# Kernel tuning notes

Measured on AMD Instinct MI355X. Metric: run time of the kernel, lower is better.

## Reference

```python
import jax, jax.numpy as jnp
import numpy as np

N_NODES, E_TOT, E_ACT = 20000, 250000, 200000
LAT, OH = 128, 128
M0, M1, M2 = 64, 32, 16            # irreps_out: 64x0e + 32x1o + 16x2e
D_IR = M0 + 3 * M1 + 5 * M2        # 240
G = M1 + M2                        # gate scalars (48)
T0 = M0 + G                        # tp m=0 scalar channels (112)
I0, I1, I2 = 3 * M0, 3 * M1, 3 * M2  # tp input muls (center|edge|neighbor)


def _split(x, m0, m1, m2):
    e = x.shape[0]
    return (x[:, :m0],
            x[:, m0:m0 + 3 * m1].reshape(e, m1, 3),
            x[:, m0 + 3 * m1:].reshape(e, m2, 5))


def _merge(s0, s1, s2):
    e = s0.shape[0]
    return jnp.concatenate([s0, s1.reshape(e, -1), s2.reshape(e, -1)], axis=-1)


def _mlp(x, ws, bs):
    for i, (w, b) in enumerate(zip(ws, bs)):
        x = x @ w + b
        if i < len(ws) - 1:
            x = jax.nn.silu(x)
    return x


def _forward(latents, node_features, edge_features, cutoff_coeffs, edge_one_hot,
             wigner_D1, wigner_D2,
             W0, W1r, W1i, W2r, W2i, Gw, Gb,
             P0, P0b, P1, P2, Ew, Eb, ln_g, ln_b,
             A1, A1b, A2, A2b, A3, A3b,
             B1, B1b, B2, B2b, B3, B3b,
             O0, O1, O2,
             edge_index, active_edges):
    ec = edge_index[0][active_edges]
    en = edge_index[1][active_edges]
    # gather node features per edge (equivariant_norm_type='none' -> identity norms)
    nc0, nc1, nc2 = _split(node_features[ec], M0, M1, M2)
    ef0, ef1, ef2 = _split(edge_features, M0, M1, M2)
    nn0, nn1, nn2 = _split(node_features[en], M0, M1, M2)
    x0 = jnp.concatenate([nc0, ef0, nn0], -1)   # [E,192]
    x1 = jnp.concatenate([nc1, ef1, nn1], 1)    # [E,96,3]
    x2 = jnp.concatenate([nc2, ef2, nn2], 1)    # [E,48,5]
    lat_a = latents[active_edges]
    # --- SO(2) linear: rotate into edge frame, per-m mixing, latent gains, rotate back ---
    r1 = jnp.einsum('eij,euj->eui', wigner_D1, x1)
    r2 = jnp.einsum('eij,euj->eui', wigner_D2, x2)
    in0 = jnp.concatenate([x0, r1[:, :, 1], r2[:, :, 2]], -1)   # m=0 [E,336]
    o_m0 = in0 @ W0.T                                           # [E,160]
    ip1 = jnp.concatenate([r1[:, :, 2], r2[:, :, 3]], -1)       # m=+1 [E,144]
    im1 = jnp.concatenate([r1[:, :, 0], r2[:, :, 1]], -1)       # m=-1
    op1 = ip1 @ W1r.T - im1 @ W1i.T                             # [E,48]
    on1 = ip1 @ W1i.T + im1 @ W1r.T
    op2 = r2[:, :, 4] @ W2r.T - r2[:, :, 0] @ W2i.T             # [E,16]
    on2 = r2[:, :, 4] @ W2i.T + r2[:, :, 0] @ W2r.T
    g = lat_a @ Gw + Gb                                         # per-edge gains [E,224]
    o_m0 = o_m0 * g[:, :160]
    g1 = g[:, 160:208]; g2 = g[:, 208:224]
    op1 = op1 * g1; on1 = on1 * g1; op2 = op2 * g2; on2 = on2 * g2
    y0 = o_m0[:, :T0]
    y1 = jnp.stack([on1[:, :M1], o_m0[:, T0:T0 + M1], op1[:, :M1]], -1)          # [E,32,3]
    y2 = jnp.stack([on2, on1[:, M1:], o_m0[:, T0 + M1:], op1[:, M1:], op2], -1)  # [E,16,5]
    y1 = jnp.einsum('eji,euj->eui', wigner_D1, y1)
    y2 = jnp.einsum('eji,euj->eui', wigner_D2, y2)
    # --- gate activation ---
    gates = jax.nn.sigmoid(y0[:, M0:])
    z0 = jax.nn.silu(y0[:, :M0])
    z1 = y1 * gates[:, :M1, None]
    z2 = y2 * gates[:, M1:, None]
    # --- lin_post: per-l channel mixing, fan-in normalized, bias on scalars ---
    z0 = z0 @ P0.T / np.sqrt(M0) + P0b
    z1 = jnp.einsum('uv,evm->eum', P1, z1) / np.sqrt(M1)
    z2 = jnp.einsum('uv,evm->eum', P2, z2) / np.sqrt(M2)
    scalars = z0                                               # taken before weighting
    # --- E3ElementLinear: per-edge per-channel weights from latents ---
    w = lat_a @ Ew + Eb                                        # [E,112]
    z0 = z0 * w[:, :M0]
    z1 = z1 * w[:, M0:M0 + M1, None]
    z2 = z2 * w[:, M0 + M1:, None]
    new_edge = _merge(z0, z1, z2)
    # --- latent update: LN -> mlp1(ln_lat||scalars) -> mlp2(h||one_hot) -> cutoff ---
    mu = lat_a.mean(-1, keepdims=True)
    var = ((lat_a - mu) ** 2).mean(-1, keepdims=True)
    ln_lat = (lat_a - mu) * jax.lax.rsqrt(var + 1e-5) * ln_g + ln_b
    h = _mlp(jnp.concatenate([ln_lat, scalars], -1), (A1, A2, A3), (A1b, A2b, A3b))
    h = _mlp(jnp.concatenate([h, edge_one_hot], -1), (B1, B2, B3), (B1b, B2b, B3b))
    new_lat = cutoff_coeffs[active_edges][:, None] * h
    # --- residual update (res_update_params buffer = 0) ---
    u = jax.nn.sigmoid(jnp.asarray(0.0, new_edge.dtype))
    c_old = jax.lax.rsqrt(u * u + 1.0)
    c_new = u * c_old
    edge_out = c_old * edge_features + c_new * new_edge        # identity residual path
    latents_out = latents.at[active_edges].set(c_new * new_lat + c_old * lat_a)
    # --- layer one-hot tensor product (uvu with 128x0e) ---
    f0, f1, f2 = _split(edge_out, M0, M1, M2)
    s = 1.0 / np.sqrt(OH)
    t0 = f0 * (edge_one_hot @ O0.T) * s
    t1 = f1 * (edge_one_hot @ O1.T)[:, :, None] * s
    t2 = f2 * (edge_one_hot @ O2.T)[:, :, None] * s
    edge_out = edge_out + _merge(t0, t1, t2)
    return edge_out, latents_out


def setup_inputs() -> dict:
    key = jax.random.key(0)
    ks = iter(jax.random.split(key, 64))
    nrm = lambda sh, s=0.05: jax.random.normal(next(ks), sh, jnp.float32) * s
    inp = dict(
        latents=nrm((E_TOT, LAT), 1.0),
        node_features=nrm((N_NODES, D_IR), 1.0),
        edge_features=nrm((E_ACT, D_IR), 1.0),
        cutoff_coeffs=jax.random.uniform(next(ks), (E_TOT,), jnp.float32),
        edge_one_hot=jax.random.uniform(next(ks), (E_ACT, OH), jnp.float32),
        wigner_D1=nrm((E_ACT, 3, 3), 0.5),
        wigner_D2=nrm((E_ACT, 5, 5), 0.3),
        W0=nrm((160, I0 + I1 + I2)), W1r=nrm((48, 144)), W1i=nrm((48, 144)),
        W2r=nrm((16, 48)), W2i=nrm((16, 48)),
        Gw=nrm((LAT, 224)), Gb=jnp.ones((224,), jnp.float32),
        P0=nrm((M0, M0)), P0b=nrm((M0,)), P1=nrm((M1, M1)), P2=nrm((M2, M2)),
        Ew=nrm((LAT, M0 + M1 + M2)), Eb=jnp.ones((M0 + M1 + M2,), jnp.float32),
        ln_g=jnp.ones((LAT,), jnp.float32), ln_b=jnp.zeros((LAT,), jnp.float32),
        A1=nrm((LAT + M0, LAT)), A1b=nrm((LAT,)),
        A2=nrm((LAT, LAT)), A2b=nrm((LAT,)),
        A3=nrm((LAT, LAT)), A3b=nrm((LAT,)),
        B1=nrm((LAT + OH, LAT)), B1b=nrm((LAT,)),
        B2=nrm((LAT, LAT)), B2b=nrm((LAT,)),
        B3=nrm((LAT, LAT)), B3b=nrm((LAT,)),
        O0=nrm((M0, OH)), O1=nrm((M1, OH)), O2=nrm((M2, OH)),
        edge_index=jax.random.randint(next(ks), (2, E_TOT), 0, N_NODES, jnp.int32),
        active_edges=jnp.sort(jax.random.permutation(next(ks), E_TOT)[:E_ACT]).astype(jnp.int32),
    )
    return inp


def reference(latents, node_features, edge_features, cutoff_coeffs, edge_one_hot,
              wigner_D1, wigner_D2,
              W0, W1r, W1i, W2r, W2i, Gw, Gb,
              P0, P0b, P1, P2, Ew, Eb, ln_g, ln_b,
              A1, A1b, A2, A2b, A3, A3b,
              B1, B1b, B2, B2b, B3, B3b,
              O0, O1, O2, edge_index, active_edges):
    return _forward(latents, node_features, edge_features, cutoff_coeffs, edge_one_hot,
                    wigner_D1, wigner_D2,
                    W0, W1r, W1i, W2r, W2i, Gw, Gb,
                    P0, P0b, P1, P2, Ew, Eb, ln_g, ln_b,
                    A1, A1b, A2, A2b, A3, A3b,
                    B1, B1b, B2, B2b, B3, B3b,
                    O0, O1, O2, edge_index, active_edges)
```

## Files before the change

### kernel.cpp

```cpp
#include <hip/hip_runtime.h>

typedef unsigned short us_t;
typedef short bf16x8 __attribute__((ext_vector_type(8)));
typedef float f32x4 __attribute__((ext_vector_type(4)));

#define E_ACT 200000
#define E_TOT 250000
#define DIR   240
#define C_OLD 0.8944271909999159f
#define C_NEW 0.4472135954999579f
#define S_OH  0.08838834764831845f

#define WO_W0   0
#define WO_W1P  56320
#define WO_W1M  70144
#define WO_W2P  83968
#define WO_W2M  85504
#define WO_GW   87040
#define WO_EW   115712
#define WO_A1   130048
#define WO_A2   154624
#define WO_A3   171008
#define WO_B1   187392
#define WO_B2   220160
#define WO_B3   236544
#define WO_O0   252928
#define WO_O1   261120
#define WO_O2   265216
#define WO_P0T  267264
#define WO_P1T  271360
#define WO_P2T  272384
#define W_TOTAL 272896

__device__ __forceinline__ float b2f(us_t u) { return __uint_as_float(((unsigned)u) << 16); }
__device__ __forceinline__ us_t f2b(float f) {
    unsigned x = __float_as_uint(f);
    return (us_t)((x + 0x7fffu + ((x >> 16) & 1u)) >> 16);
}
__device__ __forceinline__ float sigm(float x) { return 1.0f / (1.0f + __expf(-x)); }

#define MFMA(a,b,c) __builtin_amdgcn_mfma_f32_16x16x32_bf16((a),(b),(c),0,0,0)

__global__ __launch_bounds__(256) void prep_kernel(
    const float* __restrict__ W0, const float* __restrict__ W1r, const float* __restrict__ W1i,
    const float* __restrict__ W2r, const float* __restrict__ W2i,
    const float* __restrict__ Gw, const float* __restrict__ Ew,
    const float* __restrict__ A1, const float* __restrict__ A2, const float* __restrict__ A3,
    const float* __restrict__ B1, const float* __restrict__ B2, const float* __restrict__ B3,
    const float* __restrict__ O0, const float* __restrict__ O1, const float* __restrict__ O2,
    const float* __restrict__ P0w, const float* __restrict__ P1w, const float* __restrict__ P2w,
    us_t* __restrict__ wb)
{
    int idx = blockIdx.x * 256 + threadIdx.x;
    if (idx >= W_TOTAL) return;
    float v;
    if (idx < WO_W1P) {
        int r = idx, n = r / 352, k = r % 352;
        v = (k < 336) ? W0[n * 336 + k] : 0.f;
    } else if (idx < WO_W1M) {
        int r = idx - WO_W1P, n = r / 288, k = r % 288;
        v = (k < 144) ? W1r[n * 144 + k] : -W1i[n * 144 + (k - 144)];
    } else if (idx < WO_W2P) {
        int r = idx - WO_W1M, n = r / 288, k = r % 288;
        v = (k < 144) ? W1i[n * 144 + k] : W1r[n * 144 + (k - 144)];
    } else if (idx < WO_W2M) {
        int r = idx - WO_W2P, n = r / 96, k = r % 96;
        v = (k < 48) ? W2r[n * 48 + k] : -W2i[n * 48 + (k - 48)];
    } else if (idx < WO_GW) {
        int r = idx - WO_W2M, n = r / 96, k = r % 96;
        v = (k < 48) ? W2i[n * 48 + k] : W2r[n * 48 + (k - 48)];
    } else if (idx < WO_EW) {
        int r = idx - WO_GW, n = r / 128, k = r % 128;
        v = Gw[k * 224 + n];
    } else if (idx < WO_A1) {
        int r = idx - WO_EW, n = r / 128, k = r % 128;
        v = Ew[k * 112 + n];
    } else if (idx < WO_A2) {
        int r = idx - WO_A1, n = r / 192, k = r % 192;
        v = A1[k * 128 + n];
    } else if (idx < WO_A3) {
        int r = idx - WO_A2, n = r / 128, k = r % 128;
        v = A2[k * 128 + n];
    } else if (idx < WO_B1) {
        int r = idx - WO_A3, n = r / 128, k = r % 128;
        v = A3[k * 128 + n];
    } else if (idx < WO_B2) {
        int r = idx - WO_B1, n = r / 256, k = r % 256;
        v = B1[k * 128 + n];
    } else if (idx < WO_B3) {
        int r = idx - WO_B2, n = r / 128, k = r % 128;
        v = B2[k * 128 + n];
    } else if (idx < WO_O0) {
        int r = idx - WO_B3, n = r / 128, k = r % 128;
        v = B3[k * 128 + n];
    } else if (idx < WO_O1) {
        v = O0[idx - WO_O0];
    } else if (idx < WO_O2) {
        v = O1[idx - WO_O1];
    } else if (idx < WO_P0T) {
        v = O2[idx - WO_O2];
    } else if (idx < WO_P1T) {
        v = P0w[idx - WO_P0T];
    } else if (idx < WO_P2T) {
        v = P1w[idx - WO_P1T];
    } else {
        int r = idx - WO_P2T, n = r / 32, k = r % 32;
        v = (k < 16) ? P2w[n * 16 + k] : 0.f;
    }
    wb[idx] = f2b(v);
}

__device__ __forceinline__ void lat_fetch_a(const float* __restrict__ latents,
                                            const int* __restrict__ aes_l,
                                            int lane, bf16x8 a[4])
{
    const int r = lane & 15, g = lane >> 4;
    const float* lp = latents + (size_t)aes_l[r] * 128 + g * 8;
    #pragma unroll
    for (int ks = 0; ks < 4; ++ks) {
        float4 v0 = *(const float4*)(lp + ks * 32);
        float4 v1 = *(const float4*)(lp + ks * 32 + 4);
        bf16x8 av;
        av[0] = (short)f2b(v0.x); av[1] = (short)f2b(v0.y);
        av[2] = (short)f2b(v0.z); av[3] = (short)f2b(v0.w);
        av[4] = (short)f2b(v1.x); av[5] = (short)f2b(v1.y);
        av[6] = (short)f2b(v1.z); av[7] = (short)f2b(v1.w);
        a[ks] = av;
    }
}

__device__ __forceinline__ void gemmW0g32(
    const us_t* __restrict__ in0s, const us_t* __restrict__ wbase,
    const bf16x8 lA[4], const bf16x8 lB[4], const float* __restrict__ Gb,
    int nt, us_t* __restrict__ om0g, int lane)
{
    const int r = lane & 15, g = lane >> 4;
    f32x4 wa = {0.f,0.f,0.f,0.f}, wb = wa, ga = wa, gb = wa;
    const us_t* apA = in0s + r * 360 + g * 8;
    const us_t* apB = in0s + (16 + r) * 360 + g * 8;
    const us_t* wp  = wbase + WO_W0 + (size_t)(nt * 16 + r) * 352 + g * 8;
    #pragma unroll
    for (int ks = 0; ks < 11; ++ks) {
        bf16x8 b = *(const bf16x8*)(wp + ks * 32);
        wa = MFMA(*(const bf16x8*)(apA + ks * 32), b, wa);
        wb = MFMA(*(const bf16x8*)(apB + ks * 32), b, wb);
    }
    const us_t* gp = wbase + WO_GW + (size_t)(nt * 16 + r) * 128 + g * 8;
    #pragma unroll
    for (int ks = 0; ks < 4; ++ks) {
        bf16x8 b = *(const bf16x8*)(gp + ks * 32);
        ga = MFMA(lA[ks], b, ga);
        gb = MFMA(lB[ks], b, gb);
    }
    float bi = Gb[nt * 16 + r];
    #pragma unroll
    for (int i = 0; i < 4; ++i) {
        int eA = g * 4 + i, eB = 16 + g * 4 + i;
        om0g[eA * 162 + nt * 16 + r] = f2b(wa[i] * (ga[i] + bi));
        om0g[eB * 162 + nt * 16 + r] = f2b(wb[i] * (gb[i] + bi));
    }
}

__device__ __forceinline__ void gemmW1g32(
    const us_t* __restrict__ cact1, const us_t* __restrict__ wbase,
    const bf16x8 lA[4], const bf16x8 lB[4], const float* __restrict__ Gb,
    int j, us_t* __restrict__ cp1g, us_t* __restrict__ cn1g, int lane)
{
    const int r = lane & 15, g = lane >> 4;
    f32x4 pa = {0.f,0.f,0.f,0.f}, pb = pa, ma = pa, mb = pa, ga = pa, gb = pa;
    const us_t* apA = cact1 + r * 296 + g * 8;
    const us_t* apB = cact1 + (16 + r) * 296 + g * 8;
    const us_t* wpP = wbase + WO_W1P + (size_t)(j * 16 + r) * 288 + g * 8;
    const us_t* wpM = wbase + WO_W1M + (size_t)(j * 16 + r) * 288 + g * 8;
    #pragma unroll
    for (int ks = 0; ks < 9; ++ks) {
        bf16x8 aA = *(const bf16x8*)(apA + ks * 32);
        bf16x8 aB = *(const bf16x8*)(apB + ks * 32);
        bf16x8 bP = *(const bf16x8*)(wpP + ks * 32);
        bf16x8 bM = *(const bf16x8*)(wpM + ks * 32);
        pa = MFMA(aA, bP, pa); pb = MFMA(aB, bP, pb);
        ma = MFMA(aA, bM, ma); mb = MFMA(aB, bM, mb);
    }
    const us_t* gp = wbase + WO_GW + (size_t)(160 + j * 16 + r) * 128 + g * 8;
    #pragma unroll
    for (int ks = 0; ks < 4; ++ks) {
        bf16x8 b = *(const bf16x8*)(gp + ks * 32);
        ga = MFMA(lA[ks], b, ga);
        gb = MFMA(lB[ks], b, gb);
    }
    float bi = Gb[160 + j * 16 + r];
    #pragma unroll
    for (int i = 0; i < 4; ++i) {
        int eA = g * 4 + i, eB = 16 + g * 4 + i;
        float gA = ga[i] + bi, gB = gb[i] + bi;
        cp1g[eA * 50 + j * 16 + r] = f2b(pa[i] * gA);
        cn1g[eA * 50 + j * 16 + r] = f2b(ma[i] * gA);
        cp1g[eB * 50 + j * 16 + r] = f2b(pb[i] * gB);
        cn1g[eB * 50 + j * 16 + r] = f2b(mb[i] * gB);
    }
}

__device__ __forceinline__ void gemmW2g32(
    const us_t* __restrict__ cact2, const us_t* __restrict__ wbase,
    const bf16x8 lA[4], const bf16x8 lB[4], const float* __restrict__ Gb,
    us_t* __restrict__ cp2g, us_t* __restrict__ cn2g, int lane)
{
    const int r = lane & 15, g = lane >> 4;
    f32x4 pa = {0.f,0.f,0.f,0.f}, pb = pa, ma = pa, mb = pa, ga = pa, gb = pa;
    const us_t* apA = cact2 + r * 104 + g * 8;
    const us_t* apB = cact2 + (16 + r) * 104 + g * 8;
    const us_t* wpP = wbase + WO_W2P + (size_t)r * 96 + g * 8;
    const us_t* wpM = wbase + WO_W2M + (size_t)r * 96 + g * 8;
    #pragma unroll
    for (int ks = 0; ks < 3; ++ks) {
        bf16x8 aA = *(const bf16x8*)(apA + ks * 32);
        bf16x8 aB = *(const bf16x8*)(apB + ks * 32);
        bf16x8 bP = *(const bf16x8*)(wpP + ks * 32);
        bf16x8 bM = *(const bf16x8*)(wpM + ks * 32);
        pa = MFMA(aA, bP, pa); pb = MFMA(aB, bP, pb);
        ma = MFMA(aA, bM, ma); mb = MFMA(aB, bM, mb);
    }
    const us_t* gp = wbase + WO_GW + (size_t)(208 + r) * 128 + g * 8;
    #pragma unroll
    for (int ks = 0; ks < 4; ++ks) {
        bf16x8 b = *(const bf16x8*)(gp + ks * 32);
        ga = MFMA(lA[ks], b, ga);
        gb = MFMA(lB[ks], b, gb);
    }
    float bi = Gb[208 + r];
    #pragma unroll
    for (int i = 0; i < 4; ++i) {
        int eA = g * 4 + i, eB = 16 + g * 4 + i;
        float gA = ga[i] + bi, gB = gb[i] + bi;
        cp2g[eA * 18 + r] = f2b(pa[i] * gA);
        cn2g[eA * 18 + r] = f2b(ma[i] * gA);
        cp2g[eB * 18 + r] = f2b(pb[i] * gB);
        cn2g[eB * 18 + r] = f2b(mb[i] * gB);
    }
}

__device__ __forceinline__ void lat_gemmE32(
    const bf16x8 lA[4], const bf16x8 lB[4],
    const us_t* __restrict__ wgt, const float* __restrict__ bias,
    int nt, us_t* __restrict__ wl, int lane)
{
    const int r = lane & 15, g = lane >> 4;
    f32x4 aA = {0.f,0.f,0.f,0.f}, aB = aA;
    const us_t* wp = wgt + (size_t)(nt * 16 + r) * 128 + g * 8;
    #pragma unroll
    for (int ks = 0; ks < 4; ++ks) {
        bf16x8 b = *(const bf16x8*)(wp + ks * 32);
        aA = MFMA(lA[ks], b, aA);
        aB = MFMA(lB[ks], b, aB);
    }
    float bi = bias[nt * 16 + r];
    #pragma unroll
    for (int i = 0; i < 4; ++i) {
        int eA = g * 4 + i, eB = 16 + g * 4 + i;
        wl[eA * 120 + nt * 16 + r] = f2b(aA[i] + bi);
        wl[eB * 120 + nt * 16 + r] = f2b(aB[i] + bi);
    }
}

template<int KS>
__device__ __forceinline__ void pgemm32(const us_t* __restrict__ actbase, int as,
                                        const us_t* __restrict__ wgt, int kp, int lane,
                                        f32x4& accA, f32x4& accB)
{
    const int r = lane & 15, g = lane >> 4;
    const us_t* apA = actbase + r * as + g * 8;
    const us_t* apB = actbase + (16 + r) * as + g * 8;
    const us_t* wp = wgt + (size_t)r * kp + g * 8;
    #pragma unroll
    for (int ks = 0; ks < KS; ++ks) {
        bf16x8 b = *(const bf16x8*)(wp + ks * 32);
        accA = MFMA(*(const bf16x8*)(apA + ks * 32), b, accA);
        accB = MFMA(*(const bf16x8*)(apB + ks * 32), b, accB);
    }
}

__global__ __launch_bounds__(256, 2) void k1_kernel(
    const float* __restrict__ latents,
    const float* __restrict__ node_features,
    const float* __restrict__ edge_features,
    const float* __restrict__ wD1,
    const float* __restrict__ wD2,
    const float* __restrict__ Gb,  const float* __restrict__ Eb,
    const float* __restrict__ P0b,
    const int* __restrict__ edge_index, const int* __restrict__ active_edges,
    const us_t* __restrict__ wbase,
    us_t* __restrict__ ne_ws, us_t* __restrict__ scal_ws)
{
    __shared__ __align__(16) char smem[80640];
    us_t* in0s  = (us_t*)(smem);
    us_t* cact1 = (us_t*)(smem + 23040);
    us_t* cact2 = (us_t*)(smem + 41984);
    float* D1l  = (float*)(smem + 48640);
    float* D2l  = (float*)(smem + 50176);
    int*   aes  = (int*)(smem + 53760);
    us_t* om0g  = (us_t*)(smem + 53888);
    us_t* cp1g  = (us_t*)(smem + 64256);
    us_t* cn1g  = (us_t*)(smem + 67456);
    us_t* cp2g  = (us_t*)(smem + 70656);
    us_t* cn2g  = (us_t*)(smem + 71808);
    us_t* wl    = (us_t*)(smem + 72960);
    us_t* z0l   = (us_t*)(smem);
    us_t* z1l   = (us_t*)(smem + 4608);
    us_t* z2l   = (us_t*)(smem + 11264);

    const int t  = threadIdx.x;
    const int e0 = blockIdx.x * 32;

    #pragma unroll
    for (int ep = 0; ep < 2; ++ep) {
        const int e = (t >> 4) + 16 * ep, l = t & 15;
        const int eg = e0 + e;
        const int ae = active_edges[eg];
        const int ec = edge_index[ae];
        const int en = edge_index[E_TOT + ae];
        if (l == 0) aes[e] = ae;

        float v1  = (l < 9) ? wD1[(size_t)eg * 9 + l] : 0.f;
        float v2a = wD2[(size_t)eg * 25 + l];
        float v2b = (l < 9) ? wD2[(size_t)eg * 25 + 16 + l] : 0.f;
        if (l < 9) D1l[e * 12 + l] = v1;
        D2l[e * 28 + l] = v2a;
        if (l < 9) D2l[e * 28 + 16 + l] = v2b;

        float d1[9], d2[25];
        #pragma unroll
        for (int i = 0; i < 9; ++i)  d1[i] = __shfl(v1, i, 16);
        #pragma unroll
        for (int i = 0; i < 16; ++i) d2[i] = __shfl(v2a, i, 16);
        #pragma unroll
        for (int i = 0; i < 9; ++i)  d2[16 + i] = __shfl(v2b, i, 16);

        const float* pc = node_features + (size_t)ec * DIR;
        const float* pe = edge_features + (size_t)eg * DIR;
        const float* pn = node_features + (size_t)en * DIR;
        us_t* in0 = in0s + e * 360;
        us_t* c1  = cact1 + e * 296;
        us_t* c2  = cact2 + e * 104;

        #pragma unroll
        for (int j = 0; j < 4; ++j) {
            int i = l + 16 * j;
            in0[i]       = f2b(pc[i]);
            in0[64 + i]  = f2b(pe[i]);
            in0[128 + i] = f2b(pn[i]);
        }
        in0[336 + l] = 0;

        #pragma unroll
        for (int jj = 0; jj < 6; ++jj) {
            int u = l + 16 * jj;
            int uu = u & 31;
            const float* sp = (u < 32 ? pc : (u < 64 ? pe : pn)) + 64 + uu * 3;
            float x0 = sp[0], x1 = sp[1], x2 = sp[2];
            float r0 = d1[0] * x0 + d1[1] * x1 + d1[2] * x2;
            float r1 = d1[3] * x0 + d1[4] * x1 + d1[5] * x2;
            float r2 = d1[6] * x0 + d1[7] * x1 + d1[8] * x2;
            c1[144 + u]  = f2b(r0);
            in0[192 + u] = f2b(r1);
            c1[u]        = f2b(r2);
        }
        #pragma unroll
        for (int jj = 0; jj < 3; ++jj) {
            int u = l + 16 * jj;
            int uu = u & 15;
            const float* sp = (u < 16 ? pc : (u < 32 ? pe : pn)) + 160 + uu * 5;
            float x0 = sp[0], x1 = sp[1], x2 = sp[2], x3 = sp[3], x4 = sp[4];
            float r[5];
            #pragma unroll
            for (int i = 0; i < 5; ++i)
                r[i] = d2[i * 5 + 0] * x0 + d2[i * 5 + 1] * x1 + d2[i * 5 + 2] * x2
                     + d2[i * 5 + 3] * x3 + d2[i * 5 + 4] * x4;
            c2[48 + u]   = f2b(r[0]);
            c1[240 + u]  = f2b(r[1]);
            in0[288 + u] = f2b(r[2]);
            c1[96 + u]   = f2b(r[3]);
            c2[u]        = f2b(r[4]);
        }
    }
    __syncthreads();

    {
        const int lane = t & 63, w = t >> 6;
        bf16x8 lA[4], lB[4];
        lat_fetch_a(latents, aes, lane, lA);
        lat_fetch_a(latents, aes + 16, lane, lB);
        if (w == 0) {
            gemmW0g32(in0s, wbase, lA, lB, Gb, 0, om0g, lane);
            gemmW0g32(in0s, wbase, lA, lB, Gb, 1, om0g, lane);
            gemmW0g32(in0s, wbase, lA, lB, Gb, 2, om0g, lane);
            gemmW1g32(cact1, wbase, lA, lB, Gb, 0, cp1g, cn1g, lane);
        } else if (w == 1) {
            gemmW0g32(in0s, wbase, lA, lB, Gb, 3, om0g, lane);
            gemmW0g32(in0s, wbase, lA, lB, Gb, 4, om0g, lane);
            gemmW0g32(in0s, wbase, lA, lB, Gb, 5, om0g, lane);
            gemmW1g32(cact1, wbase, lA, lB, Gb, 1, cp1g, cn1g, lane);
        } else if (w == 2) {
            gemmW0g32(in0s, wbase, lA, lB, Gb, 6, om0g, lane);
            gemmW0g32(in0s, wbase, lA, lB, Gb, 7, om0g, lane);
            gemmW0g32(in0s, wbase, lA, lB, Gb, 8, om0g, lane);
            gemmW1g32(cact1, wbase, lA, lB, Gb, 2, cp1g, cn1g, lane);
        } else {
            gemmW0g32(in0s, wbase, lA, lB, Gb, 9, om0g, lane);
            gemmW2g32(cact2, wbase, lA, lB, Gb, cp2g, cn2g, lane);
            #pragma unroll
            for (int nt = 0; nt < 7; ++nt)
                lat_gemmE32(lA, lB, wbase + WO_EW, Eb, nt, wl, lane);
        }
    }
    __syncthreads();

    #pragma unroll
    for (int ep = 0; ep < 2; ++ep) {
        const int e = (t >> 4) + 16 * ep, l = t & 15;
        const float* D1e = D1l + e * 12;
        const float* D2e = D2l + e * 28;
        #pragma unroll
        for (int uu = 0; uu < 2; ++uu) {
            int u = l + uu * 16;
            float j0 = b2f(cn1g[e * 50 + u]);
            float j1 = b2f(om0g[e * 162 + 112 + u]);
            float j2 = b2f(cp1g[e * 50 + u]);
            float gate = sigm(b2f(om0g[e * 162 + 64 + u]));
            #pragma unroll
            for (int i = 0; i < 3; ++i) {
                float yr = D1e[0 * 3 + i] * j0 + D1e[1 * 3 + i] * j1 + D1e[2 * 3 + i] * j2;
                z1l[e * 104 + i * 32 + u] = f2b(yr * gate);
            }
        }
        {
            int u = l;
            float j0 = b2f(cn2g[e * 18 + u]);
            float j1 = b2f(cn1g[e * 50 + 32 + u]);
            float j2 = b2f(om0g[e * 162 + 144 + u]);
            float j3 = b2f(cp1g[e * 50 + 32 + u]);
            float j4 = b2f(cp2g[e * 18 + u]);
            float gate = sigm(b2f(om0g[e * 162 + 96 + u]));
            #pragma unroll
            for (int i = 0; i < 5; ++i) {
                float yr = D2e[0 * 5 + i] * j0 + D2e[1 * 5 + i] * j1 + D2e[2 * 5 + i] * j2
                         + D2e[3 * 5 + i] * j3 + D2e[4 * 5 + i] * j4;
                z2l[e * 168 + i * 32 + u] = f2b(yr * gate);
                z2l[e * 168 + i * 32 + 16 + u] = 0;
            }
        }
        #pragma unroll
        for (int ii = 0; ii < 4; ++ii) {
            int c = l + 16 * ii;
            float v = b2f(om0g[e * 162 + c]);
            z0l[e * 72 + c] = f2b(v * sigm(v));
        }
    }
    __syncthreads();

    {
        const int lane = t & 63, w = t >> 6;
        const int r = lane & 15, g = lane >> 4;
        const float sc1 = 0.17677669529663687f;
        if (w < 2) {
            #pragma unroll
            for (int jj = 0; jj < 2; ++jj) {
                int nt = 2 * w + jj;
                f32x4 aA = {0.f,0.f,0.f,0.f}, aB = aA;
                pgemm32<2>(z0l, 72, wbase + WO_P0T + nt * 16 * 64, 64, lane, aA, aB);
                int n = nt * 16 + r;
                float bi = P0b[n];
                #pragma unroll
                for (int i = 0; i < 4; ++i) {
                    int eA = g * 4 + i, eB = 16 + g * 4 + i;
                    float zA = aA[i] * 0.125f + bi;
                    float zB = aB[i] * 0.125f + bi;
                    scal_ws[(size_t)(e0 + eA) * 64 + n] = f2b(zA);
                    scal_ws[(size_t)(e0 + eB) * 64 + n] = f2b(zB);
                    ne_ws[(size_t)(e0 + eA) * 240 + n] = f2b(zA * b2f(wl[eA * 120 + n]));
                    ne_ws[(size_t)(e0 + eB) * 240 + n] = f2b(zB * b2f(wl[eB * 120 + n]));
                }
            }
        } else if (w == 2) {
            #pragma unroll
            for (int m = 0; m < 3; ++m) {
                #pragma unroll
                for (int nt = 0; nt < 2; ++nt) {
                    f32x4 aA = {0.f,0.f,0.f,0.f}, aB = aA;
                    pgemm32<1>(z1l + m * 32, 104, wbase + WO_P1T + nt * 16 * 32, 32,
                               lane, aA, aB);
                    int u = nt * 16 + r;
                    #pragma unroll
                    for (int i = 0; i < 4; ++i) {
                        int eA = g * 4 + i, eB = 16 + g * 4 + i;
                        ne_ws[(size_t)(e0 + eA) * 240 + 64 + u * 3 + m] =
                            f2b(aA[i] * sc1 * b2f(wl[eA * 120 + 64 + u]));
                        ne_ws[(size_t)(e0 + eB) * 240 + 64 + u * 3 + m] =
                            f2b(aB[i] * sc1 * b2f(wl[eB * 120 + 64 + u]));
                    }
                }
            }
        } else if (w == 3) {
            #pragma unroll
            for (int m = 0; m < 5; ++m) {
                f32x4 aA = {0.f,0.f,0.f,0.f}, aB = aA;
                pgemm32<1>(z2l + m * 32, 168, wbase + WO_P2T, 32, lane, aA, aB);
                int u = r;
                #pragma unroll
                for (int i = 0; i < 4; ++i) {
                    int eA = g * 4 + i, eB = 16 + g * 4 + i;
                    ne_ws[(size_t)(e0 + eA) * 240 + 160 + u * 5 + m] =
                        f2b(aA[i] * 0.25f * b2f(wl[eA * 120 + 96 + u]));
                    ne_ws[(size_t)(e0 + eB) * 240 + 160 + u * 5 + m] =
                        f2b(aB[i] * 0.25f * b2f(wl[eB * 120 + 96 + u]));
                }
            }
        }
    }
}

template<int KS, bool SILU>
__device__ __forceinline__ void mlayer(
    const us_t* __restrict__ actA, const us_t* __restrict__ actB, int split, int as,
    const us_t* __restrict__ wgt, int kp, const float* __restrict__ bias,
    us_t* __restrict__ out, int os, int lane, int w)
{
    const int r = lane & 15, g = lane >> 4;
    const int n0 = 2 * w * 16, n1 = n0 + 16;
    f32x4 a00 = {0.f,0.f,0.f,0.f}, a01 = a00, a10 = a00, a11 = a00;
    const us_t* wp0 = wgt + (size_t)(n0 + r) * kp + g * 8;
    const us_t* wp1 = wgt + (size_t)(n1 + r) * kp + g * 8;
    #pragma unroll
    for (int ks = 0; ks < KS; ++ks) {
        const us_t* ab = (ks < split) ? (actA + ks * 32) : (actB + (ks - split) * 32);
        bf16x8 f0 = *(const bf16x8*)(ab + r * as + g * 8);
        bf16x8 f1 = *(const bf16x8*)(ab + (16 + r) * as + g * 8);
        bf16x8 b0 = *(const bf16x8*)(wp0 + ks * 32);
        bf16x8 b1 = *(const bf16x8*)(wp1 + ks * 32);
        a00 = MFMA(f0, b0, a00); a01 = MFMA(f0, b1, a01);
        a10 = MFMA(f1, b0, a10); a11 = MFMA(f1, b1, a11);
    }
    float bi0 = bias[n0 + r], bi1 = bias[n1 + r];
    #pragma unroll
    for (int i = 0; i < 4; ++i) {
        int eA = g * 4 + i, eB = 16 + g * 4 + i;
        float v;
        v = a00[i] + bi0; if (SILU) v *= sigm(v); out[eA * os + n0 + r] = f2b(v);
        v = a01[i] + bi1; if (SILU) v *= sigm(v); out[eA * os + n1 + r] = f2b(v);
        v = a10[i] + bi0; if (SILU) v *= sigm(v); out[eB * os + n0 + r] = f2b(v);
        v = a11[i] + bi1; if (SILU) v *= sigm(v); out[eB * os + n1 + r] = f2b(v);
    }
}

__global__ __launch_bounds__(256, 3) void k2_kernel(
    const float* __restrict__ latents, const float* __restrict__ cutoff,
    const float* __restrict__ one_hot,
    const float* __restrict__ ln_g, const float* __restrict__ ln_b,
    const float* __restrict__ A1b, const float* __restrict__ A2b, const float* __restrict__ A3b,
    const float* __restrict__ B1b, const float* __restrict__ B2b, const float* __restrict__ B3b,
    const int* __restrict__ active_edges,
    const us_t* __restrict__ wbase,
    const us_t* __restrict__ scal_ws, us_t* __restrict__ ohw_ws,
    float* __restrict__ out_lat)
{
    __shared__ __align__(16) char smem[39424];
    us_t* x_lds = (us_t*)(smem);
    us_t* h_a   = (us_t*)(smem + 12800);
    us_t* h_b   = (us_t*)(smem + 21504);
    us_t* ohl   = (us_t*)(smem + 30208);
    int*  aes_l = (int*)(smem + 38912);
    float* cut_l= (float*)(smem + 39040);

    const int t  = threadIdx.x;
    const int e0 = blockIdx.x * 32;
    const int lane = t & 63, w = t >> 6;

    {
        int ee = t >> 3, l8 = t & 7;
        int ae = active_edges[e0 + ee];
        if (l8 == 0) { aes_l[ee] = ae; cut_l[ee] = cutoff[ae]; }
        const float* lp = latents + (size_t)ae * 128 + l8 * 16;
        float xs[16];
        #pragma unroll
        for (int q = 0; q < 4; ++q) {
            float4 v = *(const float4*)(lp + q * 4);
            xs[q * 4 + 0] = v.x; xs[q * 4 + 1] = v.y;
            xs[q * 4 + 2] = v.z; xs[q * 4 + 3] = v.w;
        }
        float s1 = 0.f, s2 = 0.f;
        #pragma unroll
        for (int i = 0; i < 16; ++i) { s1 += xs[i]; s2 += xs[i] * xs[i]; }
        #pragma unroll
        for (int off = 1; off < 8; off <<= 1) {
            s1 += __shfl_xor(s1, off, 8);
            s2 += __shfl_xor(s2, off, 8);
        }
        float mu  = s1 * (1.f / 128.f);
        float var = s2 * (1.f / 128.f) - mu * mu;
        float rstd = rsqrtf(var + 1e-5f);
        #pragma unroll
        for (int i = 0; i < 16; ++i) {
            int li = l8 * 16 + i;
            x_lds[ee * 200 + li] = f2b((xs[i] - mu) * rstd * ln_g[li] + ln_b[li]);
        }
    }
    for (int idx = t; idx < 32 * 16; idx += 256) {
        int ee = idx >> 4, j = idx & 15;
        *(ushort4*)&x_lds[ee * 200 + 128 + j * 4] =
            *(const ushort4*)&scal_ws[(size_t)(e0 + ee) * 64 + j * 4];
    }
    for (int idx = t; idx < 32 * 32; idx += 256) {
        int ee = idx >> 5, j = idx & 31;
        float4 ov = *(const float4*)&one_hot[(size_t)(e0 + ee) * 128 + j * 4];
        ushort4 s; s.x = f2b(ov.x); s.y = f2b(ov.y); s.z = f2b(ov.z); s.w = f2b(ov.w);
        *(ushort4*)&ohl[ee * 136 + j * 4] = s;
    }
    __syncthreads();

    mlayer<6, true>(x_lds, x_lds, 6, 200, wbase + WO_A1, 192, A1b, h_a, 136, lane, w);
    __syncthreads();
    mlayer<4, true>(h_a, h_a, 4, 136, wbase + WO_A2, 128, A2b, h_b, 136, lane, w);
    __syncthreads();
    mlayer<4, false>(h_b, h_b, 4, 136, wbase + WO_A3, 128, A3b, h_a, 136, lane, w);
    __syncthreads();
    mlayer<8, true>(h_a, ohl, 4, 136, wbase + WO_B1, 256, B1b, h_b, 136, lane, w);
    __syncthreads();
    mlayer<4, true>(h_b, h_b, 4, 136, wbase + WO_B2, 128, B2b, h_a, 136, lane, w);
    __syncthreads();
    {
        const int r = lane & 15, g = lane >> 4;
        const int n0 = 2 * w * 16, n1 = n0 + 16;
        f32x4 a00 = {0.f,0.f,0.f,0.f}, a01 = a00, a10 = a00, a11 = a00;
        const us_t* wp0 = wbase + WO_B3 + (size_t)(n0 + r) * 128 + g * 8;
        const us_t* wp1 = wbase + WO_B3 + (size_t)(n1 + r) * 128 + g * 8;
        #pragma unroll
        for (int ks = 0; ks < 4; ++ks) {
            bf16x8 f0 = *(const bf16x8*)(h_a + ks * 32 + r * 136 + g * 8);
            bf16x8 f1 = *(const bf16x8*)(h_a + ks * 32 + (16 + r) * 136 + g * 8);
            bf16x8 b0 = *(const bf16x8*)(wp0 + ks * 32);
            bf16x8 b1 = *(const bf16x8*)(wp1 + ks * 32);
            a00 = MFMA(f0, b0, a00); a01 = MFMA(f0, b1, a01);
            a10 = MFMA(f1, b0, a10); a11 = MFMA(f1, b1, a11);
        }
        float bi0 = B3b[n0 + r], bi1 = B3b[n1 + r];
        #pragma unroll
        for (int i = 0; i < 4; ++i) {
            int eA = g * 4 + i, eB = 16 + g * 4 + i;
            int aeA = aes_l[eA], aeB = aes_l[eB];
            float cA = C_NEW * cut_l[eA], cB = C_NEW * cut_l[eB];
            float* oA = out_lat + (size_t)aeA * 128;
            float* oB = out_lat + (size_t)aeB * 128;
            const float* lA = latents + (size_t)aeA * 128;
            const float* lB = latents + (size_t)aeB * 128;
            oA[n0 + r] = cA * (a00[i] + bi0) + C_OLD * lA[n0 + r];
            oA[n1 + r] = cA * (a01[i] + bi1) + C_OLD * lA[n1 + r];
            oB[n0 + r] = cB * (a10[i] + bi0) + C_OLD * lB[n0 + r];
            oB[n1 + r] = cB * (a11[i] + bi1) + C_OLD * lB[n1 + r];
        }
    }

    {
        const int r = lane & 15, g = lane >> 4;
        const int cnt = (w == 3) ? 1 : 2;
        #pragma unroll
        for (int ii = 0; ii < 2; ++ii) {
            if (ii >= cnt) break;
            int nt = (ii == 0) ? w : w + 4;
            const us_t* wb2 = (nt < 4) ? (wbase + WO_O0 + (size_t)nt * 16 * 128)
                            : (nt < 6) ? (wbase + WO_O1 + (size_t)(nt - 4) * 16 * 128)
                                       : (wbase + WO_O2);
            f32x4 c0 = {0.f,0.f,0.f,0.f}, c1 = c0;
            const us_t* wp = wb2 + (size_t)r * 128 + g * 8;
            #pragma unroll
            for (int ks = 0; ks < 4; ++ks) {
                bf16x8 f0 = *(const bf16x8*)(ohl + ks * 32 + r * 136 + g * 8);
                bf16x8 f1 = *(const bf16x8*)(ohl + ks * 32 + (16 + r) * 136 + g * 8);
                bf16x8 b = *(const bf16x8*)(wp + ks * 32);
                c0 = MFMA(f0, b, c0); c1 = MFMA(f1, b, c1);
            }
            int n = nt * 16 + r;
            #pragma unroll
            for (int i = 0; i < 4; ++i) {
                int eA = e0 + g * 4 + i, eB = e0 + 16 + g * 4 + i;
                ohw_ws[(size_t)eA * 112 + n] = f2b(c0[i]);
                ohw_ws[(size_t)eB * 112 + n] = f2b(c1[i]);
            }
        }
    }
}

__global__ __launch_bounds__(256) void kfin_kernel(
    const float* __restrict__ edge_features, const us_t* __restrict__ ne_ws,
    const us_t* __restrict__ ohw_ws, float* __restrict__ out_edge)
{
    int idx = blockIdx.x * 256 + threadIdx.x;
    if (idx >= E_ACT * 60) return;
    int e = idx / 60;
    int c0 = (idx - e * 60) * 4;
    float4 ef = *(const float4*)&edge_features[(size_t)e * 240 + c0];
    ushort4 nv = *(const ushort4*)&ne_ws[(size_t)e * 240 + c0];
    float nef[4] = {b2f(nv.x), b2f(nv.y), b2f(nv.z), b2f(nv.w)};
    float eff[4] = {ef.x, ef.y, ef.z, ef.w};
    float4 ov;
    float* op = &ov.x;
    #pragma unroll
    for (int j = 0; j < 4; ++j) {
        int c = c0 + j;
        int o;
        if (c < 64)       o = c;
        else if (c < 160) o = 64 + (c - 64) / 3;
        else              o = 96 + (c - 160) / 5;
        float ohv = b2f(ohw_ws[(size_t)e * 112 + o]);
        op[j] = (C_OLD * eff[j] + C_NEW * nef[j]) * (1.f + S_OH * ohv);
    }
    *(float4*)&out_edge[(size_t)e * 240 + c0] = ov;
}

extern "C" void kernel_launch(void* const* d_in, const int* in_sizes, int n_in,
                              void* d_out, int out_size, void* d_ws, size_t ws_size,
                              hipStream_t stream)
{
    const float* latents  = (const float*)d_in[0];
    const float* node_f   = (const float*)d_in[1];
    const float* edge_f   = (const float*)d_in[2];
    const float* cutoff   = (const float*)d_in[3];
    const float* one_hot  = (const float*)d_in[4];
    const float* wD1      = (const float*)d_in[5];
    const float* wD2      = (const float*)d_in[6];
    const float* W0       = (const float*)d_in[7];
    const float* W1r      = (const float*)d_in[8];
    const float* W1i      = (const float*)d_in[9];
    const float* W2r      = (const float*)d_in[10];
    const float* W2i      = (const float*)d_in[11];
    const float* Gw       = (const float*)d_in[12];
    const float* Gb       = (const float*)d_in[13];
    const float* P0w      = (const float*)d_in[14];
    const float* P0b      = (const float*)d_in[15];
    const float* P1w      = (const float*)d_in[16];
    const float* P2w      = (const float*)d_in[17];
    const float* Ew       = (const float*)d_in[18];
    const float* Eb       = (const float*)d_in[19];
    const float* ln_g     = (const float*)d_in[20];
    const float* ln_b     = (const float*)d_in[21];
    const float* A1       = (const float*)d_in[22];
    const float* A1b      = (const float*)d_in[23];
    const float* A2       = (const float*)d_in[24];
    const float* A2b      = (const float*)d_in[25];
    const float* A3       = (const float*)d_in[26];
    const float* A3b      = (const float*)d_in[27];
    const float* B1       = (const float*)d_in[28];
    const float* B1b      = (const float*)d_in[29];
    const float* B2       = (const float*)d_in[30];
    const float* B2b      = (const float*)d_in[31];
    const float* B3       = (const float*)d_in[32];
    const float* B3b      = (const float*)d_in[33];
    const float* O0       = (const float*)d_in[34];
    const float* O1       = (const float*)d_in[35];
    const float* O2       = (const float*)d_in[36];
    const int* edge_index = (const int*)d_in[37];
    const int* act_e      = (const int*)d_in[38];

    float* out_edge = (float*)d_out;
    float* out_lat  = out_edge + (size_t)E_ACT * DIR;

    us_t* ne_ws   = (us_t*)d_ws;
    us_t* ohw_ws  = ne_ws + (size_t)E_ACT * DIR;
    us_t* scal_ws = ohw_ws + (size_t)E_ACT * 112;
    us_t* wbase   = scal_ws + (size_t)E_ACT * 64;

    prep_kernel<<<dim3((W_TOTAL + 255) / 256), dim3(256), 0, stream>>>(
        W0, W1r, W1i, W2r, W2i, Gw, Ew, A1, A2, A3, B1, B2, B3,
        O0, O1, O2, P0w, P1w, P2w, wbase);

    hipMemcpyAsync(out_lat, latents, (size_t)E_TOT * 128 * sizeof(float),
                   hipMemcpyDeviceToDevice, stream);

    k1_kernel<<<dim3(E_ACT / 32), dim3(256), 0, stream>>>(
        latents, node_f, edge_f, wD1, wD2, Gb, Eb, P0b,
        edge_index, act_e, wbase, ne_ws, scal_ws);

    k2_kernel<<<dim3(E_ACT / 32), dim3(256), 0, stream>>>(
        latents, cutoff, one_hot, ln_g, ln_b,
        A1b, A2b, A3b, B1b, B2b, B3b,
        act_e, wbase, scal_ws, ohw_ws, out_lat);

    kfin_kernel<<<dim3((E_ACT * 60 + 255) / 256), dim3(256), 0, stream>>>(
        edge_f, ne_ws, ohw_ws, out_edge);
}
```

Before: 713.6 us.

## Tile latent MLP at 64 edges per block and copy only inactive latent rows

The latent MLP kernel now handles 64 edges per block instead of 32. Each wave reuses its weight fragments across four row groups, which doubles MFMA work per weight load but needs twice the LDS and lowers occupancy to 2 blocks. The full-tensor device copy of latents into the output is replaced by a kernel that binary-searches the active edge list and copies only inactive rows, so rows that k2 overwrites are no longer written twice. The binary search adds per-thread scattered reads of the index array.

New measurement: 718.3 us. Within noise of the previous version (+0.7%).

```diff
diff --git a/kernel.cpp b/kernel.cpp
--- a/kernel.cpp
+++ b/kernel.cpp
@@ -110,6 +110,27 @@
     wb[idx] = f2b(v);
 }
 
+__global__ __launch_bounds__(256) void kcopy_kernel(
+    const float* __restrict__ latents, const int* __restrict__ act,
+    float* __restrict__ out_lat)
+{
+    int idx = blockIdx.x * 256 + threadIdx.x;
+    if (idx >= E_TOT * 16) return;
+    int row = idx >> 4, part = idx & 15;
+    int lo = 0, hi = E_ACT;
+    while (lo < hi) {
+        int mid = (lo + hi) >> 1;
+        if (act[mid] < row) lo = mid + 1; else hi = mid;
+    }
+    bool active = (lo < E_ACT) && (act[lo] == row);
+    if (!active) {
+        const float4* src = (const float4*)&latents[(size_t)row * 128 + part * 8];
+        float4* dst = (float4*)&out_lat[(size_t)row * 128 + part * 8];
+        dst[0] = src[0];
+        dst[1] = src[1];
+    }
+}
+
 __device__ __forceinline__ void lat_fetch_a(const float* __restrict__ latents,
                                             const int* __restrict__ aes_l,
                                             int lane, bf16x8 a[4])
@@ -519,39 +540,47 @@
 }
 
 template<int KS, bool SILU>
-__device__ __forceinline__ void mlayer(
+__device__ __forceinline__ void mlayer64(
     const us_t* __restrict__ actA, const us_t* __restrict__ actB, int split, int as,
     const us_t* __restrict__ wgt, int kp, const float* __restrict__ bias,
     us_t* __restrict__ out, int os, int lane, int w)
 {
     const int r = lane & 15, g = lane >> 4;
     const int n0 = 2 * w * 16, n1 = n0 + 16;
-    f32x4 a00 = {0.f,0.f,0.f,0.f}, a01 = a00, a10 = a00, a11 = a00;
+    f32x4 a0e0 = {0.f,0.f,0.f,0.f}, a0e1 = a0e0, a0e2 = a0e0, a0e3 = a0e0;
+    f32x4 a1e0 = a0e0, a1e1 = a0e0, a1e2 = a0e0, a1e3 = a0e0;
     const us_t* wp0 = wgt + (size_t)(n0 + r) * kp + g * 8;
     const us_t* wp1 = wgt + (size_t)(n1 + r) * kp + g * 8;
     #pragma unroll
     for (int ks = 0; ks < KS; ++ks) {
         const us_t* ab = (ks < split) ? (actA + ks * 32) : (actB + (ks - split) * 32);
-        bf16x8 f0 = *(const bf16x8*)(ab + r * as + g * 8);
-        bf16x8 f1 = *(const bf16x8*)(ab + (16 + r) * as + g * 8);
         bf16x8 b0 = *(const bf16x8*)(wp0 + ks * 32);
         bf16x8 b1 = *(const bf16x8*)(wp1 + ks * 32);
-        a00 = MFMA(f0, b0, a00); a01 = MFMA(f0, b1, a01);
-        a10 = MFMA(f1, b0, a10); a11 = MFMA(f1, b1, a11);
+        bf16x8 f0 = *(const bf16x8*)(ab + (r)      * as + g * 8);
+        bf16x8 f1 = *(const bf16x8*)(ab + (16 + r) * as + g * 8);
+        bf16x8 f2 = *(const bf16x8*)(ab + (32 + r) * as + g * 8);
+        bf16x8 f3 = *(const bf16x8*)(ab + (48 + r) * as + g * 8);
+        a0e0 = MFMA(f0, b0, a0e0); a1e0 = MFMA(f0, b1, a1e0);
+        a0e1 = MFMA(f1, b0, a0e1); a1e1 = MFMA(f1, b1, a1e1);
+        a0e2 = MFMA(f2, b0, a0e2); a1e2 = MFMA(f2, b1, a1e2);
+        a0e3 = MFMA(f3, b0, a0e3); a1e3 = MFMA(f3, b1, a1e3);
     }
     float bi0 = bias[n0 + r], bi1 = bias[n1 + r];
-    #pragma unroll
-    for (int i = 0; i < 4; ++i) {
-        int eA = g * 4 + i, eB = 16 + g * 4 + i;
-        float v;
-        v = a00[i] + bi0; if (SILU) v *= sigm(v); out[eA * os + n0 + r] = f2b(v);
-        v = a01[i] + bi1; if (SILU) v *= sigm(v); out[eA * os + n1 + r] = f2b(v);
-        v = a10[i] + bi0; if (SILU) v *= sigm(v); out[eB * os + n0 + r] = f2b(v);
-        v = a11[i] + bi1; if (SILU) v *= sigm(v); out[eB * os + n1 + r] = f2b(v);
-    }
-}
-
-__global__ __launch_bounds__(256, 3) void k2_kernel(
+    f32x4 A0[4] = {a0e0, a0e1, a0e2, a0e3};
+    f32x4 A1[4] = {a1e0, a1e1, a1e2, a1e3};
+    #pragma unroll
+    for (int eg = 0; eg < 4; ++eg) {
+        #pragma unroll
+        for (int i = 0; i < 4; ++i) {
+            int e = eg * 16 + g * 4 + i;
+            float v;
+            v = A0[eg][i] + bi0; if (SILU) v *= sigm(v); out[e * os + n0 + r] = f2b(v);
+            v = A1[eg][i] + bi1; if (SILU) v *= sigm(v); out[e * os + n1 + r] = f2b(v);
+        }
+    }
+}
+
+__global__ __launch_bounds__(256, 2) void k2_kernel(
     const float* __restrict__ latents, const float* __restrict__ cutoff,
     const float* __restrict__ one_hot,
     const float* __restrict__ ln_g, const float* __restrict__ ln_b,
@@ -562,53 +591,53 @@
     const us_t* __restrict__ scal_ws, us_t* __restrict__ ohw_ws,
     float* __restrict__ out_lat)
 {
-    __shared__ __align__(16) char smem[39424];
+    __shared__ __align__(16) char smem[78336];
     us_t* x_lds = (us_t*)(smem);
-    us_t* h_a   = (us_t*)(smem + 12800);
-    us_t* h_b   = (us_t*)(smem + 21504);
-    us_t* ohl   = (us_t*)(smem + 30208);
-    int*  aes_l = (int*)(smem + 38912);
-    float* cut_l= (float*)(smem + 39040);
+    us_t* h_a   = (us_t*)(smem + 25600);
+    us_t* h_b   = (us_t*)(smem + 43008);
+    us_t* ohl   = (us_t*)(smem + 60416);
+    int*  aes_l = (int*)(smem + 77824);
+    float* cut_l= (float*)(smem + 78080);
 
     const int t  = threadIdx.x;
-    const int e0 = blockIdx.x * 32;
+    const int e0 = blockIdx.x * 64;
     const int lane = t & 63, w = t >> 6;
 
     {
-        int ee = t >> 3, l8 = t & 7;
+        int ee = t >> 2, l4 = t & 3;
         int ae = active_edges[e0 + ee];
-        if (l8 == 0) { aes_l[ee] = ae; cut_l[ee] = cutoff[ae]; }
-        const float* lp = latents + (size_t)ae * 128 + l8 * 16;
-        float xs[16];
-        #pragma unroll
-        for (int q = 0; q < 4; ++q) {
+        if (l4 == 0) { aes_l[ee] = ae; cut_l[ee] = cutoff[ae]; }
+        const float* lp = latents + (size_t)ae * 128 + l4 * 32;
+        float xs[32];
+        #pragma unroll
+        for (int q = 0; q < 8; ++q) {
             float4 v = *(const float4*)(lp + q * 4);
             xs[q * 4 + 0] = v.x; xs[q * 4 + 1] = v.y;
             xs[q * 4 + 2] = v.z; xs[q * 4 + 3] = v.w;
         }
         float s1 = 0.f, s2 = 0.f;
         #pragma unroll
-        for (int i = 0; i < 16; ++i) { s1 += xs[i]; s2 += xs[i] * xs[i]; }
-        #pragma unroll
-        for (int off = 1; off < 8; off <<= 1) {
-            s1 += __shfl_xor(s1, off, 8);
-            s2 += __shfl_xor(s2, off, 8);
+        for (int i = 0; i < 32; ++i) { s1 += xs[i]; s2 += xs[i] * xs[i]; }
+        #pragma unroll
+        for (int off = 1; off < 4; off <<= 1) {
+            s1 += __shfl_xor(s1, off, 4);
+            s2 += __shfl_xor(s2, off, 4);
         }
         float mu  = s1 * (1.f / 128.f);
         float var = s2 * (1.f / 128.f) - mu * mu;
         float rstd = rsqrtf(var + 1e-5f);
         #pragma unroll
-        for (int i = 0; i < 16; ++i) {
-            int li = l8 * 16 + i;
+        for (int i = 0; i < 32; ++i) {
+            int li = l4 * 32 + i;
             x_lds[ee * 200 + li] = f2b((xs[i] - mu) * rstd * ln_g[li] + ln_b[li]);
         }
     }
-    for (int idx = t; idx < 32 * 16; idx += 256) {
+    for (int idx = t; idx < 64 * 16; idx += 256) {
         int ee = idx >> 4, j = idx & 15;
         *(ushort4*)&x_lds[ee * 200 + 128 + j * 4] =
             *(const ushort4*)&scal_ws[(size_t)(e0 + ee) * 64 + j * 4];
     }
-    for (int idx = t; idx < 32 * 32; idx += 256) {
+    for (int idx = t; idx < 64 * 32; idx += 256) {
         int ee = idx >> 5, j = idx & 31;
         float4 ov = *(const float4*)&one_hot[(size_t)(e0 + ee) * 128 + j * 4];
         ushort4 s; s.x = f2b(ov.x); s.y = f2b(ov.y); s.z = f2b(ov.z); s.w = f2b(ov.w);
@@ -616,45 +645,51 @@
     }
     __syncthreads();
 
-    mlayer<6, true>(x_lds, x_lds, 6, 200, wbase + WO_A1, 192, A1b, h_a, 136, lane, w);
+    mlayer64<6, true>(x_lds, x_lds, 6, 200, wbase + WO_A1, 192, A1b, h_a, 136, lane, w);
     __syncthreads();
-    mlayer<4, true>(h_a, h_a, 4, 136, wbase + WO_A2, 128, A2b, h_b, 136, lane, w);
+    mlayer64<4, true>(h_a, h_a, 4, 136, wbase + WO_A2, 128, A2b, h_b, 136, lane, w);
     __syncthreads();
-    mlayer<4, false>(h_b, h_b, 4, 136, wbase + WO_A3, 128, A3b, h_a, 136, lane, w);
+    mlayer64<4, false>(h_b, h_b, 4, 136, wbase + WO_A3, 128, A3b, h_a, 136, lane, w);
     __syncthreads();
-    mlayer<8, true>(h_a, ohl, 4, 136, wbase + WO_B1, 256, B1b, h_b, 136, lane, w);
+    mlayer64<8, true>(h_a, ohl, 4, 136, wbase + WO_B1, 256, B1b, h_b, 136, lane, w);
     __syncthreads();
-    mlayer<4, true>(h_b, h_b, 4, 136, wbase + WO_B2, 128, B2b, h_a, 136, lane, w);
+    mlayer64<4, true>(h_b, h_b, 4, 136, wbase + WO_B2, 128, B2b, h_a, 136, lane, w);
     __syncthreads();
     {
         const int r = lane & 15, g = lane >> 4;
         const int n0 = 2 * w * 16, n1 = n0 + 16;
-        f32x4 a00 = {0.f,0.f,0.f,0.f}, a01 = a00, a10 = a00, a11 = a00;
+        f32x4 a0e0 = {0.f,0.f,0.f,0.f}, a0e1 = a0e0, a0e2 = a0e0, a0e3 = a0e0;
+        f32x4 a1e0 = a0e0, a1e1 = a0e0, a1e2 = a0e0, a1e3 = a0e0;
         const us_t* wp0 = wbase + WO_B3 + (size_t)(n0 + r) * 128 + g * 8;
         const us_t* wp1 = wbase + WO_B3 + (size_t)(n1 + r) * 128 + g * 8;
         #pragma unroll
         for (int ks = 0; ks < 4; ++ks) {
-            bf16x8 f0 = *(const bf16x8*)(h_a + ks * 32 + r * 136 + g * 8);
-            bf16x8 f1 = *(const bf16x8*)(h_a + ks * 32 + (16 + r) * 136 + g * 8);
             bf16x8 b0 = *(const bf16x8*)(wp0 + ks * 32);
             bf16x8 b1 = *(const bf16x8*)(wp1 + ks * 32);
-            a00 = MFMA(f0, b0, a00); a01 = MFMA(f0, b1, a01);
-            a10 = MFMA(f1, b0, a10); a11 = MFMA(f1, b1, a11);
+            bf16x8 f0 = *(const bf16x8*)(h_a + ks * 32 + (r)      * 136 + g * 8);
+            bf16x8 f1 = *(const bf16x8*)(h_a + ks * 32 + (16 + r) * 136 + g * 8);
+            bf16x8 f2 = *(const bf16x8*)(h_a + ks * 32 + (32 + r) * 136 + g * 8);
+            bf16x8 f3 = *(const bf16x8*)(h_a + ks * 32 + (48 + r) * 136 + g * 8);
+            a0e0 = MFMA(f0, b0, a0e0); a1e0 = MFMA(f0, b1, a1e0);
+            a0e1 = MFMA(f1, b0, a0e1); a1e1 = MFMA(f1, b1, a1e1);
+            a0e2 = MFMA(f2, b0, a0e2); a1e2 = MFMA(f2, b1, a1e2);
+            a0e3 = MFMA(f3, b0, a0e3); a1e3 = MFMA(f3, b1, a1e3);
         }
         float bi0 = B3b[n0 + r], bi1 = B3b[n1 + r];
-        #pragma unroll
-        for (int i = 0; i < 4; ++i) {
-            int eA = g * 4 + i, eB = 16 + g * 4 + i;
-            int aeA = aes_l[eA], aeB = aes_l[eB];
-            float cA = C_NEW * cut_l[eA], cB = C_NEW * cut_l[eB];
-            float* oA = out_lat + (size_t)aeA * 128;
-            float* oB = out_lat + (size_t)aeB * 128;
-            const float* lA = latents + (size_t)aeA * 128;
-            const float* lB = latents + (size_t)aeB * 128;
-            oA[n0 + r] = cA * (a00[i] + bi0) + C_OLD * lA[n0 + r];
-            oA[n1 + r] = cA * (a01[i] + bi1) + C_OLD * lA[n1 + r];
-            oB[n0 + r] = cB * (a10[i] + bi0) + C_OLD * lB[n0 + r];
-            oB[n1 + r] = cB * (a11[i] + bi1) + C_OLD * lB[n1 + r];
+        f32x4 A0[4] = {a0e0, a0e1, a0e2, a0e3};
+        f32x4 A1[4] = {a1e0, a1e1, a1e2, a1e3};
+        #pragma unroll
+        for (int eg = 0; eg < 4; ++eg) {
+            #pragma unroll
+            for (int i = 0; i < 4; ++i) {
+                int e = eg * 16 + g * 4 + i;
+                int ae = aes_l[e];
+                float c = C_NEW * cut_l[e];
+                float* o = out_lat + (size_t)ae * 128;
+                const float* lt = latents + (size_t)ae * 128;
+                o[n0 + r] = c * (A0[eg][i] + bi0) + C_OLD * lt[n0 + r];
+                o[n1 + r] = c * (A1[eg][i] + bi1) + C_OLD * lt[n1 + r];
+            }
         }
     }
 
@@ -668,21 +703,27 @@
             const us_t* wb2 = (nt < 4) ? (wbase + WO_O0 + (size_t)nt * 16 * 128)
                             : (nt < 6) ? (wbase + WO_O1 + (size_t)(nt - 4) * 16 * 128)
                                        : (wbase + WO_O2);
-            f32x4 c0 = {0.f,0.f,0.f,0.f}, c1 = c0;
+            f32x4 c0 = {0.f,0.f,0.f,0.f}, c1 = c0, c2 = c0, c3 = c0;
             const us_t* wp = wb2 + (size_t)r * 128 + g * 8;
             #pragma unroll
             for (int ks = 0; ks < 4; ++ks) {
-                bf16x8 f0 = *(const bf16x8*)(ohl + ks * 32 + r * 136 + g * 8);
+                bf16x8 b = *(const bf16x8*)(wp + ks * 32);
+                bf16x8 f0 = *(const bf16x8*)(ohl + ks * 32 + (r)      * 136 + g * 8);
                 bf16x8 f1 = *(const bf16x8*)(ohl + ks * 32 + (16 + r) * 136 + g * 8);
-                bf16x8 b = *(const bf16x8*)(wp + ks * 32);
+                bf16x8 f2 = *(const bf16x8*)(ohl + ks * 32 + (32 + r) * 136 + g * 8);
+                bf16x8 f3 = *(const bf16x8*)(ohl + ks * 32 + (48 + r) * 136 + g * 8);
                 c0 = MFMA(f0, b, c0); c1 = MFMA(f1, b, c1);
+                c2 = MFMA(f2, b, c2); c3 = MFMA(f3, b, c3);
             }
             int n = nt * 16 + r;
-            #pragma unroll
-            for (int i = 0; i < 4; ++i) {
-                int eA = e0 + g * 4 + i, eB = e0 + 16 + g * 4 + i;
-                ohw_ws[(size_t)eA * 112 + n] = f2b(c0[i]);
-                ohw_ws[(size_t)eB * 112 + n] = f2b(c1[i]);
+            f32x4 C[4] = {c0, c1, c2, c3};
+            #pragma unroll
+            for (int eg = 0; eg < 4; ++eg) {
+                #pragma unroll
+                for (int i = 0; i < 4; ++i) {
+                    int e = e0 + eg * 16 + g * 4 + i;
+                    ohw_ws[(size_t)e * 112 + n] = f2b(C[eg][i]);
+                }
             }
         }
     }
@@ -771,14 +812,14 @@
         W0, W1r, W1i, W2r, W2i, Gw, Ew, A1, A2, A3, B1, B2, B3,
         O0, O1, O2, P0w, P1w, P2w, wbase);
 
-    hipMemcpyAsync(out_lat, latents, (size_t)E_TOT * 128 * sizeof(float),
-                   hipMemcpyDeviceToDevice, stream);
-
     k1_kernel<<<dim3(E_ACT / 32), dim3(256), 0, stream>>>(
         latents, node_f, edge_f, wD1, wD2, Gb, Eb, P0b,
         edge_index, act_e, wbase, ne_ws, scal_ws);
 
-    k2_kernel<<<dim3(E_ACT / 32), dim3(256), 0, stream>>>(
+    kcopy_kernel<<<dim3((E_TOT * 16 + 255) / 256), dim3(256), 0, stream>>>(
+        latents, act_e, out_lat);
+
+    k2_kernel<<<dim3(E_ACT / 64), dim3(256), 0, stream>>>(
         latents, cutoff, one_hot, ln_g, ln_b,
         A1b, A2b, A3b, B1b, B2b, B3b,
         act_e, wbase, scal_ws, ohw_ws, out_lat);
```
